# Kernel optimization log

Measured on AMD Instinct MI355X. Metric: run time of the kernel, lower is better.

Reference implementation:

```python
import jax, jax.numpy as jnp
import numpy as np

S, D, H = 1024, 512, 4
DK = D // H  # 128
POOL = 16
EPS = 1e-5


def _pos_encoding(seq_len, dmodel):
    pos = jnp.arange(seq_len, dtype=jnp.float32)[:, None]
    div = jnp.exp(jnp.arange(0, dmodel, 2, dtype=jnp.float32) * (-jnp.log(10000.0) / dmodel))
    ang = pos * div  # [S, D/2]
    # interleave sin/cos -> pe[:,0::2]=sin, pe[:,1::2]=cos
    return jnp.stack([jnp.sin(ang), jnp.cos(ang)], axis=-1).reshape(seq_len, dmodel)


def _layernorm(x, g, b):
    mu = jnp.mean(x, axis=-1, keepdims=True)
    var = jnp.var(x, axis=-1, keepdims=True)
    return (x - mu) * jax.lax.rsqrt(var + EPS) * g + b


def setup_inputs() -> dict:
    key = jax.random.key(0)
    ks = jax.random.split(key, 16)
    u = lambda k, shape, r: jax.random.uniform(k, shape, jnp.float32, -r, r)
    nfeature = 512
    return {
        "x": jax.random.normal(ks[0], (16, S, nfeature), jnp.float32),
        "emb_w": u(ks[1], (nfeature, D), (1.0 / nfeature) ** 0.5),
        "emb_b": u(ks[2], (D,), (1.0 / nfeature) ** 0.5),
        "WQ": u(ks[3], (H, D, DK), 0.1),
        "WK": u(ks[4], (H, D, DK), 0.1),
        "WV": u(ks[5], (H, D, DK), 0.1),
        "WO": u(ks[6], (H * DK, D), 0.1),
        "g1": jnp.ones((D,), jnp.float32),
        "b1": jnp.zeros((D,), jnp.float32),
        "l1_w": u(ks[7], (D, 4 * D), (1.0 / D) ** 0.5),
        "l1_b": u(ks[8], (4 * D,), (1.0 / D) ** 0.5),
        "l2_w": u(ks[9], (4 * D, D), (1.0 / (4 * D)) ** 0.5),
        "l2_b": u(ks[10], (D,), (1.0 / (4 * D)) ** 0.5),
        "g2": jnp.ones((D,), jnp.float32),
        "b2": jnp.zeros((D,), jnp.float32),
        "fc_w": u(ks[11], (S * (D // POOL), 2), 0.1),
        "fc_b": jnp.zeros((2,), jnp.float32),
    }


def reference(x, emb_w, emb_b, WQ, WK, WV, WO, g1, b1, l1_w, l1_b, l2_w, l2_b, g2, b2, fc_w, fc_b):
    # dropout layers are identity (eval mode)
    h = x @ emb_w + emb_b                       # [B,S,D]
    h = h.reshape(-1, S, D) + _pos_encoding(S, D)
    inp = h
    # per-head projections (hand-rolled MHA)
    Qi = jnp.einsum('bsd,hde->bhse', h, WQ)     # [B,H,S,DK]
    Ki = jnp.einsum('bsd,hde->bhse', h, WK)
    Vi = jnp.einsum('bsd,hde->bhse', h, WV)
    scores = jnp.einsum('bhse,bhte->bhst', Qi, Ki) / jnp.sqrt(jnp.float32(DK))
    attn = jax.nn.softmax(scores, axis=-1)      # [B,H,S,S] -- full attention matrix, as in source
    head = jnp.einsum('bhst,bhte->bhse', attn, Vi)  # [B,H,S,DK]
    # NOTE: source does a raw reshape [B,H,S,DK] -> [B,S,H*DK] (no transpose); replicate exactly
    out = head.reshape(-1, S, H * DK) @ WO      # [B,S,D]
    h = _layernorm(out + inp, g1, b1)
    ffn = jax.nn.relu(h @ l1_w + l1_b) @ l2_w + l2_b
    h = _layernorm(ffn + h, g2, b2)
    # MaxPool1d(16,16) over the feature dim: [B,S,512] -> [B,S,32]
    pooled = h.reshape(-1, S, D // POOL, POOL).max(axis=-1)
    logits = pooled.reshape(-1, S * (D // POOL)) @ fc_w + fc_b  # [B,2]
    return jax.nn.log_softmax(logits, axis=-1)
```

## Files before the change

### kernel.cpp

```cpp
#include <hip/hip_runtime.h>

typedef unsigned short ushortb;
typedef __attribute__((ext_vector_type(8))) short short8;
typedef __attribute__((ext_vector_type(4))) float f32x4;

__device__ __forceinline__ ushortb f2bb(float f) {
    union { float f; unsigned u; } x; x.f = f;
    unsigned r = x.u + 0x7fffu + ((x.u >> 16) & 1u);
    return (ushortb)(r >> 16);
}
__device__ __forceinline__ float bb2f(ushortb u) {
    union { unsigned u; float f; } x; x.u = ((unsigned)u) << 16; return x.f;
}

__device__ __forceinline__ unsigned pkbb(float a, float b) {
#if __has_builtin(__builtin_amdgcn_cvt_pk_bf16_f32)
    auto p = __builtin_amdgcn_cvt_pk_bf16_f32(a, b);
    unsigned u; __builtin_memcpy(&u, &p, 4);
    return u;
#else
    return (unsigned)f2bb(a) | ((unsigned)f2bb(b) << 16);
#endif
}

#if __has_builtin(__builtin_amdgcn_exp2f)
#define EXP2(x) __builtin_amdgcn_exp2f(x)
#else
#define EXP2(x) exp2f(x)
#endif

__device__ __forceinline__ void async_ld16(void* lds, const void* g) {
    __builtin_amdgcn_global_load_lds(
        (const __attribute__((address_space(1))) void*)g,
        (__attribute__((address_space(3))) void*)lds, 16, 0, 0);
}

#define EP_EMB       0
#define EP_RES       2
#define EP_BIAS_RELU 3
#define EP_BIAS_RES  4
#define EP_QKV       7

template <int EP, int BM>
__global__ __launch_bounds__(512, 2) void gemm_big(
    const ushortb* __restrict__ A, const ushortb* __restrict__ Bt,
    const float* __restrict__ bias, const ushortb* __restrict__ res,
    const float* __restrict__ pe, ushortb* __restrict__ C,
    int M, int N, int K)
{
    constexpr int MI = BM / 32;
    constexpr int CA = BM / 64;
    __shared__ ushortb sA[2][BM][64];
    __shared__ ushortb sB[2][256][64];

    const int tid = threadIdx.x;
    const int wave = tid >> 6, lane = tid & 63;
    const int quad = lane >> 4, l15 = lane & 15;
    const int row0 = blockIdx.x * BM;
    const int col0 = blockIdx.y * 256;
    const int wm = (wave >> 2) * (BM / 2);
    const int wn = (wave & 3) * 64;
    const int srl = lane >> 3, slot = lane & 7;

    f32x4 acc[MI][4];
    #pragma unroll
    for (int i = 0; i < MI; ++i)
        #pragma unroll
        for (int j = 0; j < 4; ++j) acc[i][j] = (f32x4){0.f, 0.f, 0.f, 0.f};

    auto stage = [&](int b, int k0) {
        #pragma unroll
        for (int c = 0; c < CA; ++c) {
            int rbase = (wave * CA + c) * 8;
            int r = rbase + srl;
            int ka = (slot ^ ((r ^ (r >> 3)) & 7)) * 8;
            async_ld16(&sA[b][rbase][0], A + (size_t)(row0 + r) * K + k0 + ka);
        }
        #pragma unroll
        for (int c = 0; c < 4; ++c) {
            int rbase = (wave * 4 + c) * 8;
            int r = rbase + srl;
            int ka = (slot ^ ((r ^ (r >> 3)) & 7)) * 8;
            async_ld16(&sB[b][rbase][0], Bt + (size_t)(col0 + r) * K + k0 + ka);
        }
    };

    const int NT = K >> 6;
    stage(0, 0);
    stage(1, 64);
    if constexpr (BM == 256) asm volatile("s_waitcnt vmcnt(8)" ::: "memory");
    else                     asm volatile("s_waitcnt vmcnt(6)" ::: "memory");
    __builtin_amdgcn_sched_barrier(0);
    __builtin_amdgcn_s_barrier();

    for (int t = 0; t < NT; ++t) {
        const int b = t & 1;
        #pragma unroll
        for (int kc = 0; kc < 2; ++kc) {
            short8 af[MI], bf[4];
            #pragma unroll
            for (int i = 0; i < MI; ++i) {
                int m = wm + i * 16 + l15;
                af[i] = *(const short8*)&sA[b][m][(((kc * 4 + quad) ^ ((m ^ (m >> 3)) & 7))) * 8];
            }
            #pragma unroll
            for (int j = 0; j < 4; ++j) {
                int n = wn + j * 16 + l15;
                bf[j] = *(const short8*)&sB[b][n][(((kc * 4 + quad) ^ ((n ^ (n >> 3)) & 7))) * 8];
            }
            #pragma unroll
            for (int i = 0; i < MI; ++i)
                #pragma unroll
                for (int j = 0; j < 4; ++j)
                    acc[i][j] = __builtin_amdgcn_mfma_f32_16x16x32_bf16(af[i], bf[j], acc[i][j], 0, 0, 0);
        }
        if (t == NT - 1) break;
        asm volatile("s_waitcnt lgkmcnt(0)" ::: "memory");
        __builtin_amdgcn_sched_barrier(0);
        __builtin_amdgcn_s_barrier();
        if (t + 2 < NT) {
            stage(b, (t + 2) << 6);
            if constexpr (BM == 256) asm volatile("s_waitcnt vmcnt(8)" ::: "memory");
            else                     asm volatile("s_waitcnt vmcnt(6)" ::: "memory");
        } else {
            asm volatile("s_waitcnt vmcnt(0)" ::: "memory");
        }
        __builtin_amdgcn_sched_barrier(0);
        __builtin_amdgcn_s_barrier();
    }

    if constexpr (EP == EP_QKV) {
        if (col0 < 1024) {
            ushortb* dst = C + ((size_t)(col0 >> 9)) * ((size_t)M * 512);
            #pragma unroll
            for (int i = 0; i < MI; ++i)
                #pragma unroll
                for (int r = 0; r < 4; ++r) {
                    int row = row0 + wm + i * 16 + quad * 4 + r;
                    #pragma unroll
                    for (int j = 0; j < 4; ++j) {
                        int col = (col0 + wn + j * 16 + l15) & 511;
                        dst[(size_t)row * 512 + col] = f2bb(acc[i][j][r]);
                    }
                }
        } else {
            ushortb* Vt = C + (size_t)2 * M * 512;
            int bb_ = row0 >> 10;
            #pragma unroll
            for (int i = 0; i < MI; ++i) {
                int s = (row0 & 1023) + wm + i * 16 + quad * 4;
                #pragma unroll
                for (int j = 0; j < 4; ++j) {
                    int vcol = col0 + wn + j * 16 + l15 - 1024;
                    int h = vcol >> 7, e = vcol & 127;
                    uint2 v;
                    v.x = pkbb(acc[i][j][0], acc[i][j][1]);
                    v.y = pkbb(acc[i][j][2], acc[i][j][3]);
                    *(uint2*)&Vt[((size_t)((bb_ * 4 + h) * 128 + e) << 10) + s] = v;
                }
            }
        }
        return;
    }

    #pragma unroll
    for (int i = 0; i < MI; ++i) {
        #pragma unroll
        for (int r = 0; r < 4; ++r) {
            int row = row0 + wm + i * 16 + quad * 4 + r;
            #pragma unroll
            for (int j = 0; j < 4; ++j) {
                int col = col0 + wn + j * 16 + l15;
                float v = acc[i][j][r];
                if constexpr (EP == EP_EMB) {
                    v += bias[col] + pe[((row & 1023) << 9) + col];
                } else if constexpr (EP == EP_RES) {
                    v += bb2f(res[(size_t)row * N + col]);
                } else if constexpr (EP == EP_BIAS_RELU) {
                    v = fmaxf(v + bias[col], 0.0f);
                } else if constexpr (EP == EP_BIAS_RES) {
                    v += bias[col] + bb2f(res[(size_t)row * N + col]);
                }
                C[(size_t)row * N + col] = f2bb(v);
            }
        }
    }
}

__global__ __launch_bounds__(256) void conv_x(const float* __restrict__ in,
                                              ushortb* __restrict__ out)
{
    size_t i4 = (size_t)blockIdx.x * 256 + threadIdx.x;
    float4 v = *(const float4*)(in + i4 * 4);
    ushort4 o;
    o.x = f2bb(v.x); o.y = f2bb(v.y); o.z = f2bb(v.z); o.w = f2bb(v.w);
    *(ushort4*)(out + i4 * 4) = o;
}

__global__ __launch_bounds__(256) void tileT(const float* __restrict__ in,
                                             ushortb* __restrict__ out,
                                             int R, int C, float scale)
{
    __shared__ float t[64][65];
    const int tx = threadIdx.x & 63, ty = threadIdx.x >> 6;
    const int c0 = blockIdx.x * 64, r0 = blockIdx.y * 64;
    const size_t zoff = (size_t)blockIdx.z * R * C;
    #pragma unroll
    for (int i = 0; i < 16; ++i) {
        int r = ty + i * 4;
        t[r][tx] = in[zoff + (size_t)(r0 + r) * C + c0 + tx] * scale;
    }
    __syncthreads();
    #pragma unroll
    for (int i = 0; i < 16; ++i) {
        int r = ty + i * 4;
        out[zoff + (size_t)(c0 + r) * R + r0 + tx] = f2bb(t[tx][r]);
    }
}

__global__ __launch_bounds__(256) void pairT512(const float* __restrict__ emb_w,
                                                const float* __restrict__ WO,
                                                ushortb* __restrict__ embwt,
                                                ushortb* __restrict__ wot)
{
    __shared__ float t[64][65];
    const int tx = threadIdx.x & 63, ty = threadIdx.x >> 6;
    const int c0 = blockIdx.x * 64, r0 = blockIdx.y * 64;
    const float* in = blockIdx.z ? WO : emb_w;
    ushortb* out = blockIdx.z ? wot : embwt;
    #pragma unroll
    for (int i = 0; i < 16; ++i) {
        int r = ty + i * 4;
        t[r][tx] = in[(size_t)(r0 + r) * 512 + c0 + tx];
    }
    __syncthreads();
    #pragma unroll
    for (int i = 0; i < 16; ++i) {
        int r = ty + i * 4;
        out[(size_t)(c0 + r) * 512 + r0 + tx] = f2bb(t[tx][r]);
    }
}

__global__ __launch_bounds__(256) void qkvT(const float* __restrict__ WQ,
                                            const float* __restrict__ WK,
                                            const float* __restrict__ WV,
                                            ushortb* __restrict__ wqkvt,
                                            float qscale)
{
    __shared__ float t[64][65];
    const int tx = threadIdx.x & 63, ty = threadIdx.x >> 6;
    const int c0 = blockIdx.x * 64, r0 = blockIdx.y * 64;
    const int z = blockIdx.z, sel = z >> 2, zz = z & 3;
    const float* in = (sel == 0 ? WQ : (sel == 1 ? WK : WV)) + (size_t)zz * 65536;
    ushortb* out = wqkvt + (size_t)sel * 262144 + (size_t)zz * 65536;
    const float scale = (sel == 0) ? qscale : 1.0f;
    #pragma unroll
    for (int i = 0; i < 16; ++i) {
        int r = ty + i * 4;
        t[r][tx] = in[(size_t)(r0 + r) * 128 + c0 + tx] * scale;
    }
    __syncthreads();
    #pragma unroll
    for (int i = 0; i < 16; ++i) {
        int r = ty + i * 4;
        out[(size_t)(c0 + r) * 512 + r0 + tx] = f2bb(t[tx][r]);
    }
}

__global__ __launch_bounds__(256) void pe_kernel(float* __restrict__ pe)
{
    int idx = blockIdx.x * 256 + threadIdx.x;
    int s = idx >> 9, c = idx & 511;
    float div = expf((float)(c & ~1) * (-9.210340371976184f / 512.0f));
    float ang = (float)s * div;
    pe[idx] = (c & 1) ? cosf(ang) : sinf(ang);
}

__global__ __launch_bounds__(256) void attn_mfma(
    const ushortb* __restrict__ Qb, const ushortb* __restrict__ Kb,
    const ushortb* __restrict__ Vt, ushortb* __restrict__ O)
{
    __shared__ ushortb sK[2][32][128];
    __shared__ ushortb sVt[2][128][32];
    __shared__ ushortb sP[4][32][40];

    const int tid = threadIdx.x;
    const int wave = tid >> 6, lane = tid & 63;
    const int quad = lane >> 4, l15 = lane & 15;
    const int bid = blockIdx.x;
    const int bh = bid & 63, qc = bid >> 6;
    const int b = bh >> 2, h = bh & 3;
    const int q0 = qc * 128 + wave * 32;
    const size_t qk_off = ((size_t)b << 10) * 512 + h * 128;
    const ushortb* Qp = Qb + qk_off;
    const ushortb* Kp = Kb + qk_off;
    const ushortb* Vp = Vt + (((size_t)(b * 4 + h)) << 17);

    short8 qfA[4], qfB[4];
    {
        const ushortb* qa = Qp + (size_t)(q0 + l15) * 512;
        const ushortb* qb = Qp + (size_t)(q0 + 16 + l15) * 512;
        #pragma unroll
        for (int kc = 0; kc < 4; ++kc) {
            qfA[kc] = *(const short8*)(qa + kc * 32 + quad * 8);
            qfB[kc] = *(const short8*)(qb + kc * 32 + quad * 8);
        }
    }

    f32x4 oA[8], oB[8];
    #pragma unroll
    for (int dt = 0; dt < 8; ++dt) {
        oA[dt] = (f32x4){0.f, 0.f, 0.f, 0.f};
        oB[dt] = (f32x4){0.f, 0.f, 0.f, 0.f};
    }
    float lA = 0.f, lB = 0.f;

    #pragma unroll
    for (int c = 0; c < 2; ++c) {
        int seg = wave * 2 + c;
        int rk = seg * 4 + (lane >> 4);
        int ck = (lane & 15) ^ (rk & 15);
        async_ld16(&sK[0][seg * 4][0], Kp + (size_t)rk * 512 + ck * 8);
        int dv = seg * 16 + (lane >> 2);
        int cv = (lane & 3) ^ (dv & 3);
        async_ld16(&sVt[0][seg * 16][0], Vp + ((size_t)dv << 10) + cv * 8);
    }

    int buf = 0;
    for (int t0 = 0; t0 < 1024; t0 += 32) {
        __syncthreads();
        if (t0 + 32 < 1024) {
            int nb = buf ^ 1;
            #pragma unroll
            for (int c = 0; c < 2; ++c) {
                int seg = wave * 2 + c;
                int rk = seg * 4 + (lane >> 4);
                int ck = (lane & 15) ^ (rk & 15);
                async_ld16(&sK[nb][seg * 4][0], Kp + (size_t)(t0 + 32 + rk) * 512 + ck * 8);
                int dv = seg * 16 + (lane >> 2);
                int cv = (lane & 3) ^ (dv & 3);
                async_ld16(&sVt[nb][seg * 16][0], Vp + ((size_t)dv << 10) + t0 + 32 + cv * 8);
            }
        }

        f32x4 sA0 = {0,0,0,0}, sA1 = {0,0,0,0}, sB0 = {0,0,0,0}, sB1 = {0,0,0,0};
        #pragma unroll
        for (int kc = 0; kc < 4; ++kc) {
            short8 k0f = *(const short8*)&sK[buf][l15][((kc * 4 + quad) ^ l15) * 8];
            short8 k1f = *(const short8*)&sK[buf][16 + l15][((kc * 4 + quad) ^ l15) * 8];
            sA0 = __builtin_amdgcn_mfma_f32_16x16x32_bf16(k0f, qfA[kc], sA0, 0, 0, 0);
            sA1 = __builtin_amdgcn_mfma_f32_16x16x32_bf16(k1f, qfA[kc], sA1, 0, 0, 0);
            sB0 = __builtin_amdgcn_mfma_f32_16x16x32_bf16(k0f, qfB[kc], sB0, 0, 0, 0);
            sB1 = __builtin_amdgcn_mfma_f32_16x16x32_bf16(k1f, qfB[kc], sB1, 0, 0, 0);
        }

        float pA0[4], pA1[4], pB0[4], pB1[4];
        float sumA = 0.f, sumB = 0.f;
        #pragma unroll
        for (int r = 0; r < 4; ++r) {
            pA0[r] = EXP2(sA0[r]); pA1[r] = EXP2(sA1[r]);
            pB0[r] = EXP2(sB0[r]); pB1[r] = EXP2(sB1[r]);
            sumA += pA0[r] + pA1[r];
            sumB += pB0[r] + pB1[r];
        }
        lA += sumA; lB += sumB;

        uint2 w;
        w.x = pkbb(pA0[0], pA0[1]); w.y = pkbb(pA0[2], pA0[3]);
        *(uint2*)&sP[wave][l15][quad * 4] = w;
        w.x = pkbb(pA1[0], pA1[1]); w.y = pkbb(pA1[2], pA1[3]);
        *(uint2*)&sP[wave][l15][16 + quad * 4] = w;
        w.x = pkbb(pB0[0], pB0[1]); w.y = pkbb(pB0[2], pB0[3]);
        *(uint2*)&sP[wave][16 + l15][quad * 4] = w;
        w.x = pkbb(pB1[0], pB1[1]); w.y = pkbb(pB1[2], pB1[3]);
        *(uint2*)&sP[wave][16 + l15][16 + quad * 4] = w;

        short8 pfA = *(const short8*)&sP[wave][l15][quad * 8];
        short8 pfB = *(const short8*)&sP[wave][16 + l15][quad * 8];

        #pragma unroll
        for (int dt = 0; dt < 8; ++dt) {
            int d = dt * 16 + l15;
            short8 vfrag = *(const short8*)&sVt[buf][d][(quad ^ (d & 3)) * 8];
            oA[dt] = __builtin_amdgcn_mfma_f32_16x16x32_bf16(pfA, vfrag, oA[dt], 0, 0, 0);
            oB[dt] = __builtin_amdgcn_mfma_f32_16x16x32_bf16(pfB, vfrag, oB[dt], 0, 0, 0);
        }
        buf ^= 1;
    }

    lA += __shfl_xor(lA, 16); lA += __shfl_xor(lA, 32);
    lB += __shfl_xor(lB, 16); lB += __shfl_xor(lB, 32);

    const size_t obase = (((size_t)(b * 4 + h) << 10) + q0) << 7;
    #pragma unroll
    for (int r = 0; r < 4; ++r) {
        float invA = 1.0f / __shfl(lA, quad * 4 + r);
        float invB = 1.0f / __shfl(lB, quad * 4 + r);
        int qa = quad * 4 + r, qb = 16 + quad * 4 + r;
        #pragma unroll
        for (int dt = 0; dt < 8; ++dt) {
            O[obase + ((size_t)qa << 7) + dt * 16 + l15] = f2bb(oA[dt][r] * invA);
            O[obase + ((size_t)qb << 7) + dt * 16 + l15] = f2bb(oB[dt][r] * invB);
        }
    }
}

__global__ __launch_bounds__(256) void ln_kernel(const ushortb* __restrict__ in,
                                                 const float* __restrict__ g,
                                                 const float* __restrict__ bta,
                                                 ushortb* __restrict__ out)
{
    const int lane = threadIdx.x & 63, w = threadIdx.x >> 6;
    const size_t row = (size_t)blockIdx.x * 4 + w;
    const int e0 = lane * 8;
    short8 v8 = *(const short8*)(in + row * 512 + e0);
    float v[8];
    #pragma unroll
    for (int k = 0; k < 8; ++k) v[k] = bb2f((ushortb)((short*)&v8)[k]);
    float s = 0.f, sq = 0.f;
    #pragma unroll
    for (int k = 0; k < 8; ++k) { s += v[k]; sq += v[k] * v[k]; }
    #pragma unroll
    for (int o = 1; o < 64; o <<= 1) { s += __shfl_xor(s, o); sq += __shfl_xor(sq, o); }
    float mu = s * (1.0f / 512.0f);
    float var = sq * (1.0f / 512.0f) - mu * mu;
    float rstd = rsqrtf(var + 1e-5f);
    float4 g0 = *(const float4*)(g + e0),  g1 = *(const float4*)(g + e0 + 4);
    float4 b0 = *(const float4*)(bta + e0), b1 = *(const float4*)(bta + e0 + 4);
    float gg[8] = {g0.x, g0.y, g0.z, g0.w, g1.x, g1.y, g1.z, g1.w};
    float bb[8] = {b0.x, b0.y, b0.z, b0.w, b1.x, b1.y, b1.z, b1.w};
    short8 o8;
    #pragma unroll
    for (int k = 0; k < 8; ++k)
        ((short*)&o8)[k] = (short)f2bb((v[k] - mu) * rstd * gg[k] + bb[k]);
    *(short8*)(out + row * 512 + e0) = o8;
}

__global__ __launch_bounds__(256) void final_partial(const ushortb* __restrict__ ln2,
                                                     const float* __restrict__ fcw,
                                                     float* __restrict__ zbuf)
{
    const int b = blockIdx.x, chunk = blockIdx.y;
    const int tid = threadIdx.x;
    float a0 = 0.0f, a1 = 0.0f;
    #pragma unroll
    for (int t = 0; t < 8; ++t) {
        int m = chunk * 2048 + t * 256 + tid;
        int s = m >> 5, j = m & 31;
        const ushortb* p = ln2 + (((size_t)(b * 1024 + s)) << 9) + j * 16;
        float mx = -1e30f;
        #pragma unroll
        for (int e = 0; e < 16; ++e) mx = fmaxf(mx, bb2f(p[e]));
        a0 += mx * fcw[2 * m];
        a1 += mx * fcw[2 * m + 1];
    }
    __shared__ float r0[256], r1[256];
    r0[tid] = a0; r1[tid] = a1;
    __syncthreads();
    for (int o = 128; o > 0; o >>= 1) {
        if (tid < o) { r0[tid] += r0[tid + o]; r1[tid] += r1[tid + o]; }
        __syncthreads();
    }
    if (tid == 0) {
        atomicAdd(&zbuf[2 * b],     r0[0]);
        atomicAdd(&zbuf[2 * b + 1], r1[0]);
    }
}

__global__ __launch_bounds__(64) void final_logits(const float* __restrict__ zbuf,
                                                   const float* __restrict__ fcb,
                                                   float* __restrict__ out)
{
    int b = threadIdx.x;
    if (b < 16) {
        float z0 = zbuf[2 * b]     + fcb[0];
        float z1 = zbuf[2 * b + 1] + fcb[1];
        float mx = fmaxf(z0, z1);
        float lse = mx + logf(expf(z0 - mx) + expf(z1 - mx));
        out[2 * b]     = z0 - lse;
        out[2 * b + 1] = z1 - lse;
    }
}

extern "C" void kernel_launch(void* const* d_in, const int* in_sizes, int n_in,
                              void* d_out, int out_size, void* d_ws, size_t ws_size,
                              hipStream_t stream)
{
    const float* x     = (const float*)d_in[0];
    const float* emb_w = (const float*)d_in[1];
    const float* emb_b = (const float*)d_in[2];
    const float* WQ    = (const float*)d_in[3];
    const float* WK    = (const float*)d_in[4];
    const float* WV    = (const float*)d_in[5];
    const float* WO    = (const float*)d_in[6];
    const float* g1    = (const float*)d_in[7];
    const float* b1    = (const float*)d_in[8];
    const float* l1w   = (const float*)d_in[9];
    const float* l1b   = (const float*)d_in[10];
    const float* l2w   = (const float*)d_in[11];
    const float* l2b   = (const float*)d_in[12];
    const float* g2    = (const float*)d_in[13];
    const float* b2    = (const float*)d_in[14];
    const float* fcw   = (const float*)d_in[15];
    const float* fcb   = (const float*)d_in[16];
    float* out = (float*)d_out;

    char* ws = (char*)d_ws;
    const size_t Ub = (size_t)16384 * 512 * 2;
    ushortb* xb    = (ushortb*)(ws + 0 * Ub);
    ushortb* h0b   = (ushortb*)(ws + 1 * Ub);
    ushortb* Qb    = (ushortb*)(ws + 2 * Ub);
    ushortb* Kb    = (ushortb*)(ws + 3 * Ub);
    ushortb* Vt    = (ushortb*)(ws + 4 * Ub);
    ushortb* headR = (ushortb*)(ws + 5 * Ub);
    ushortb* mid   = (ushortb*)(ws + 3 * Ub);
    ushortb* r1    = xb;
    ushortb* ln1   = Qb;
    ushortb* r2    = xb;
    ushortb* ln2   = h0b;
    char* wb = ws + 7 * Ub;
    ushortb* embwt = (ushortb*)(wb);
    ushortb* wqkvt = (ushortb*)(wb + 524288);
    ushortb* wot   = (ushortb*)(wb + 2097152);
    ushortb* l1wt  = (ushortb*)(wb + 2621440);
    ushortb* l2wt  = (ushortb*)(wb + 4718592);
    float*   pe    = (float*)  (wb + 6815744);
    float*   zbuf  = (float*)  (wb + 8912896);

    const int M = 16384;
    const float qscale = 0.12753139626997592f;

    conv_x<<<8192, 256, 0, stream>>>(x, xb);
    pe_kernel<<<2048, 256, 0, stream>>>(pe);
    pairT512<<<dim3(8, 8, 2), 256, 0, stream>>>(emb_w, WO, embwt, wot);
    qkvT<<<dim3(2, 8, 12), 256, 0, stream>>>(WQ, WK, WV, wqkvt, qscale);
    tileT<<<dim3(32, 8, 1), 256, 0, stream>>>(l1w, l1wt, 512, 2048, 1.0f);
    tileT<<<dim3(8, 32, 1), 256, 0, stream>>>(l2w, l2wt, 2048, 512, 1.0f);
    hipMemsetAsync(zbuf, 0, 16 * 2 * sizeof(float), stream);

    gemm_big<EP_EMB, 128><<<dim3(M / 128, 2), 512, 0, stream>>>(
        xb, embwt, emb_b, nullptr, pe, h0b, M, 512, 512);

    gemm_big<EP_QKV, 128><<<dim3(M / 128, 6), 512, 0, stream>>>(
        h0b, wqkvt, nullptr, nullptr, nullptr, Qb, M, 1536, 512);

    attn_mfma<<<512, 256, 0, stream>>>(Qb, Kb, Vt, headR);

    gemm_big<EP_RES, 128><<<dim3(M / 128, 2), 512, 0, stream>>>(
        headR, wot, nullptr, h0b, nullptr, r1, M, 512, 512);
    ln_kernel<<<M / 4, 256, 0, stream>>>(r1, g1, b1, ln1);

    gemm_big<EP_BIAS_RELU, 256><<<dim3(M / 256, 8), 512, 0, stream>>>(
        ln1, l1wt, l1b, nullptr, nullptr, mid, M, 2048, 512);
    gemm_big<EP_BIAS_RES, 128><<<dim3(M / 128, 2), 512, 0, stream>>>(
        mid, l2wt, l2b, ln1, nullptr, r2, M, 512, 2048);
    ln_kernel<<<M / 4, 256, 0, stream>>>(r2, g2, b2, ln2);

    final_partial<<<dim3(16, 16), 256, 0, stream>>>(ln2, fcw, zbuf);
    final_logits<<<1, 64, 0, stream>>>(zbuf, fcb, out);
}
```

Baseline: 367.5 us.

## Triple-buffer LDS pipelines in GEMM and attention with one barrier per step

Moves the BM=128 GEMM path and the attention kernel from double to triple-buffered async global-to-LDS staging. The prefetch two tiles ahead is issued at the start of each iteration, so each step needs one barrier instead of two, and memory latency can overlap more compute. The attention MFMA sections are also wrapped in s_setprio raises. The cost is more LDS per block, which may lower occupancy, plus careful vmcnt accounting for the deeper pipeline.

```diff
diff --git a/kernel.cpp b/kernel.cpp
--- a/kernel.cpp
+++ b/kernel.cpp
@@ -29,6 +29,9 @@
 #define EXP2(x) exp2f(x)
 #endif
 
+#define WAITV(n) asm volatile("s_waitcnt vmcnt(" #n ")" ::: "memory")
+#define WAITL()  asm volatile("s_waitcnt lgkmcnt(0)" ::: "memory")
+
 __device__ __forceinline__ void async_ld16(void* lds, const void* g) {
     __builtin_amdgcn_global_load_lds(
         (const __attribute__((address_space(1))) void*)g,
@@ -50,8 +53,9 @@
 {
     constexpr int MI = BM / 32;
     constexpr int CA = BM / 64;
-    __shared__ ushortb sA[2][BM][64];
-    __shared__ ushortb sB[2][256][64];
+    constexpr int NBUF = (BM == 128) ? 3 : 2;
+    __shared__ ushortb sA[NBUF][BM][64];
+    __shared__ ushortb sB[NBUF][256][64];
 
     const int tid = threadIdx.x;
     const int wave = tid >> 6, lane = tid & 63;
@@ -86,47 +90,88 @@
     };
 
     const int NT = K >> 6;
-    stage(0, 0);
-    stage(1, 64);
-    if constexpr (BM == 256) asm volatile("s_waitcnt vmcnt(8)" ::: "memory");
-    else                     asm volatile("s_waitcnt vmcnt(6)" ::: "memory");
-    __builtin_amdgcn_sched_barrier(0);
-    __builtin_amdgcn_s_barrier();
-
-    for (int t = 0; t < NT; ++t) {
-        const int b = t & 1;
-        #pragma unroll
-        for (int kc = 0; kc < 2; ++kc) {
-            short8 af[MI], bf[4];
-            #pragma unroll
-            for (int i = 0; i < MI; ++i) {
-                int m = wm + i * 16 + l15;
-                af[i] = *(const short8*)&sA[b][m][(((kc * 4 + quad) ^ ((m ^ (m >> 3)) & 7))) * 8];
-            }
-            #pragma unroll
-            for (int j = 0; j < 4; ++j) {
-                int n = wn + j * 16 + l15;
-                bf[j] = *(const short8*)&sB[b][n][(((kc * 4 + quad) ^ ((n ^ (n >> 3)) & 7))) * 8];
-            }
-            #pragma unroll
-            for (int i = 0; i < MI; ++i)
-                #pragma unroll
-                for (int j = 0; j < 4; ++j)
-                    acc[i][j] = __builtin_amdgcn_mfma_f32_16x16x32_bf16(af[i], bf[j], acc[i][j], 0, 0, 0);
-        }
-        if (t == NT - 1) break;
-        asm volatile("s_waitcnt lgkmcnt(0)" ::: "memory");
+
+    if constexpr (NBUF == 3) {
+        stage(0, 0);
+        stage(1, 64);
+        WAITV(6);
         __builtin_amdgcn_sched_barrier(0);
         __builtin_amdgcn_s_barrier();
-        if (t + 2 < NT) {
-            stage(b, (t + 2) << 6);
-            if constexpr (BM == 256) asm volatile("s_waitcnt vmcnt(8)" ::: "memory");
-            else                     asm volatile("s_waitcnt vmcnt(6)" ::: "memory");
-        } else {
-            asm volatile("s_waitcnt vmcnt(0)" ::: "memory");
-        }
+        __builtin_amdgcn_sched_barrier(0);
+
+        int bc = 0;
+        for (int t = 0; t < NT; ++t) {
+            int b2 = bc + 2; if (b2 >= 3) b2 -= 3;
+            if (t + 2 < NT) stage(b2, (t + 2) << 6);
+            #pragma unroll
+            for (int kc = 0; kc < 2; ++kc) {
+                short8 af[MI], bf[4];
+                #pragma unroll
+                for (int i = 0; i < MI; ++i) {
+                    int m = wm + i * 16 + l15;
+                    af[i] = *(const short8*)&sA[bc][m][(((kc * 4 + quad) ^ ((m ^ (m >> 3)) & 7))) * 8];
+                }
+                #pragma unroll
+                for (int j = 0; j < 4; ++j) {
+                    int n = wn + j * 16 + l15;
+                    bf[j] = *(const short8*)&sB[bc][n][(((kc * 4 + quad) ^ ((n ^ (n >> 3)) & 7))) * 8];
+                }
+                #pragma unroll
+                for (int i = 0; i < MI; ++i)
+                    #pragma unroll
+                    for (int j = 0; j < 4; ++j)
+                        acc[i][j] = __builtin_amdgcn_mfma_f32_16x16x32_bf16(af[i], bf[j], acc[i][j], 0, 0, 0);
+            }
+            if (t == NT - 1) break;
+            WAITL();
+            if (t + 2 < NT) { WAITV(6); }
+            else           { WAITV(0); }
+            __builtin_amdgcn_sched_barrier(0);
+            __builtin_amdgcn_s_barrier();
+            __builtin_amdgcn_sched_barrier(0);
+            bc = bc + 1; if (bc == 3) bc = 0;
+        }
+    } else {
+        stage(0, 0);
+        stage(1, 64);
+        WAITV(8);
         __builtin_amdgcn_sched_barrier(0);
         __builtin_amdgcn_s_barrier();
+
+        for (int t = 0; t < NT; ++t) {
+            const int b = t & 1;
+            #pragma unroll
+            for (int kc = 0; kc < 2; ++kc) {
+                short8 af[MI], bf[4];
+                #pragma unroll
+                for (int i = 0; i < MI; ++i) {
+                    int m = wm + i * 16 + l15;
+                    af[i] = *(const short8*)&sA[b][m][(((kc * 4 + quad) ^ ((m ^ (m >> 3)) & 7))) * 8];
+                }
+                #pragma unroll
+                for (int j = 0; j < 4; ++j) {
+                    int n = wn + j * 16 + l15;
+                    bf[j] = *(const short8*)&sB[b][n][(((kc * 4 + quad) ^ ((n ^ (n >> 3)) & 7))) * 8];
+                }
+                #pragma unroll
+                for (int i = 0; i < MI; ++i)
+                    #pragma unroll
+                    for (int j = 0; j < 4; ++j)
+                        acc[i][j] = __builtin_amdgcn_mfma_f32_16x16x32_bf16(af[i], bf[j], acc[i][j], 0, 0, 0);
+            }
+            if (t == NT - 1) break;
+            WAITL();
+            __builtin_amdgcn_sched_barrier(0);
+            __builtin_amdgcn_s_barrier();
+            if (t + 2 < NT) {
+                stage(b, (t + 2) << 6);
+                WAITV(8);
+            } else {
+                WAITV(0);
+            }
+            __builtin_amdgcn_sched_barrier(0);
+            __builtin_amdgcn_s_barrier();
+        }
     }
 
     if constexpr (EP == EP_QKV) {
@@ -280,8 +325,8 @@
     const ushortb* __restrict__ Qb, const ushortb* __restrict__ Kb,
     const ushortb* __restrict__ Vt, ushortb* __restrict__ O)
 {
-    __shared__ ushortb sK[2][32][128];
-    __shared__ ushortb sVt[2][128][32];
+    __shared__ ushortb sK[3][32][128];
+    __shared__ ushortb sVt[3][128][32];
     __shared__ ushortb sP[4][32][40];
 
     const int tid = threadIdx.x;
@@ -315,35 +360,33 @@
     }
     float lA = 0.f, lB = 0.f;
 
-    #pragma unroll
-    for (int c = 0; c < 2; ++c) {
-        int seg = wave * 2 + c;
-        int rk = seg * 4 + (lane >> 4);
-        int ck = (lane & 15) ^ (rk & 15);
-        async_ld16(&sK[0][seg * 4][0], Kp + (size_t)rk * 512 + ck * 8);
-        int dv = seg * 16 + (lane >> 2);
-        int cv = (lane & 3) ^ (dv & 3);
-        async_ld16(&sVt[0][seg * 16][0], Vp + ((size_t)dv << 10) + cv * 8);
-    }
+    auto stage = [&](int bsel, int tt) {
+        #pragma unroll
+        for (int c = 0; c < 2; ++c) {
+            int seg = wave * 2 + c;
+            int rk = seg * 4 + (lane >> 4);
+            int ck = (lane & 15) ^ (rk & 15);
+            async_ld16(&sK[bsel][seg * 4][0], Kp + (size_t)(tt + rk) * 512 + ck * 8);
+            int dv = seg * 16 + (lane >> 2);
+            int cv = (lane & 3) ^ (dv & 3);
+            async_ld16(&sVt[bsel][seg * 16][0], Vp + ((size_t)dv << 10) + tt + cv * 8);
+        }
+    };
+
+    stage(0, 0);
+    stage(1, 32);
+    WAITV(4);
+    __builtin_amdgcn_sched_barrier(0);
+    __builtin_amdgcn_s_barrier();
+    __builtin_amdgcn_sched_barrier(0);
 
     int buf = 0;
     for (int t0 = 0; t0 < 1024; t0 += 32) {
-        __syncthreads();
-        if (t0 + 32 < 1024) {
-            int nb = buf ^ 1;
-            #pragma unroll
-            for (int c = 0; c < 2; ++c) {
-                int seg = wave * 2 + c;
-                int rk = seg * 4 + (lane >> 4);
-                int ck = (lane & 15) ^ (rk & 15);
-                async_ld16(&sK[nb][seg * 4][0], Kp + (size_t)(t0 + 32 + rk) * 512 + ck * 8);
-                int dv = seg * 16 + (lane >> 2);
-                int cv = (lane & 3) ^ (dv & 3);
-                async_ld16(&sVt[nb][seg * 16][0], Vp + ((size_t)dv << 10) + t0 + 32 + cv * 8);
-            }
-        }
+        int b2 = buf + 2; if (b2 >= 3) b2 -= 3;
+        if (t0 + 64 < 1024) stage(b2, t0 + 64);
 
         f32x4 sA0 = {0,0,0,0}, sA1 = {0,0,0,0}, sB0 = {0,0,0,0}, sB1 = {0,0,0,0};
+        __builtin_amdgcn_s_setprio(1);
         #pragma unroll
         for (int kc = 0; kc < 4; ++kc) {
             short8 k0f = *(const short8*)&sK[buf][l15][((kc * 4 + quad) ^ l15) * 8];
@@ -353,6 +396,7 @@
             sB0 = __builtin_amdgcn_mfma_f32_16x16x32_bf16(k0f, qfB[kc], sB0, 0, 0, 0);
             sB1 = __builtin_amdgcn_mfma_f32_16x16x32_bf16(k1f, qfB[kc], sB1, 0, 0, 0);
         }
+        __builtin_amdgcn_s_setprio(0);
 
         float pA0[4], pA1[4], pB0[4], pB1[4];
         float sumA = 0.f, sumB = 0.f;
@@ -378,6 +422,7 @@
         short8 pfA = *(const short8*)&sP[wave][l15][quad * 8];
         short8 pfB = *(const short8*)&sP[wave][16 + l15][quad * 8];
 
+        __builtin_amdgcn_s_setprio(1);
         #pragma unroll
         for (int dt = 0; dt < 8; ++dt) {
             int d = dt * 16 + l15;
@@ -385,7 +430,16 @@
             oA[dt] = __builtin_amdgcn_mfma_f32_16x16x32_bf16(pfA, vfrag, oA[dt], 0, 0, 0);
             oB[dt] = __builtin_amdgcn_mfma_f32_16x16x32_bf16(pfB, vfrag, oB[dt], 0, 0, 0);
         }
-        buf ^= 1;
+        __builtin_amdgcn_s_setprio(0);
+
+        if (t0 == 992) break;
+        WAITL();
+        if (t0 + 64 < 1024) { WAITV(4); }
+        else               { WAITV(0); }
+        __builtin_amdgcn_sched_barrier(0);
+        __builtin_amdgcn_s_barrier();
+        __builtin_amdgcn_sched_barrier(0);
+        buf = buf + 1; if (buf == 3) buf = 0;
     }
 
     lA += __shfl_xor(lA, 16); lA += __shfl_xor(lA, 32);
```

New measurement: 377.1 us. 2.6% more time.
